# Optimization experiments

Hardware: AMD Instinct MI355X
Metric: run time of the kernel (lower is better)

Reference implementation:

```python
import jax, jax.numpy as jnp
import numpy as np

B, S, D, H = 2, 2048, 512, 8
HD = D // H
EPS = 1e-8
SCALE = HD ** -0.5


def setup_inputs() -> dict:
    key = jax.random.key(0)
    ks = jax.random.split(key, 12)
    gene_emb = jax.random.normal(ks[0], (B, S, D), jnp.float32)
    expr_emb = jax.random.normal(ks[1], (B, S, D), jnp.float32)
    M = jax.random.randint(ks[2], (B, S, S), 0, 2).astype(jnp.float32)
    def lin(k, fan_in, fan_out):
        kw, kb = jax.random.split(k)
        bound = 1.0 / np.sqrt(fan_in)
        W = jax.random.uniform(kw, (fan_in, fan_out), jnp.float32, -bound, bound)
        b = jax.random.uniform(kb, (fan_out,), jnp.float32, -bound, bound)
        return W, b
    Wf, bf = lin(ks[3], 2 * D, D)  # fused_emb_proj
    Wq, bq = lin(ks[4], D, D)
    Wk, bk = lin(ks[5], D, D)
    Wv, bv = lin(ks[6], D, D)
    Wo, bo = lin(ks[7], D, D)
    return {"gene_emb": gene_emb, "expr_emb": expr_emb, "M": M,
            "Wf": Wf, "bf": bf, "Wq": Wq, "bq": bq, "Wk": Wk, "bk": bk,
            "Wv": Wv, "bv": bv, "Wo": Wo, "bo": bo}


def reference(gene_emb, expr_emb, M, Wf, bf, Wq, bq, Wk, bk, Wv, bv, Wo, bo):
    # fused=True, self_attention=False path: Q and K from projected concat
    fused = jnp.concatenate([gene_emb, expr_emb], axis=-1) @ Wf + bf  # [B,S,D]
    Q = (fused @ Wq + bq).reshape(B, S, H, HD)
    K = (fused @ Wk + bk).reshape(B, S, H, HD)
    V = (expr_emb @ Wv + bv).reshape(B, S, H, HD)
    scores = jnp.einsum('bqhd,bkhd->bhqk', Q, K) * SCALE  # [B,H,S,S]
    Mh = M[:, None, :, :]  # broadcast over heads
    scores = scores + jnp.where(Mh == 0, -1e9, 0.0)
    attn = jax.nn.softmax(scores, axis=-1)
    A = attn * Mh  # gated weights
    A = A / (jnp.sum(jnp.abs(A), axis=-1, keepdims=True) + EPS)  # abs-sum renorm
    out = jnp.einsum('bhqk,bkhd->bqhd', A, V).reshape(B, S, D)
    return out @ Wo + bo
```

## Files before the change

### kernel.cpp

```cpp
#include <hip/hip_runtime.h>
#include <stdint.h>
#include <math.h>

#define BB 2
#define SS 2048
#define DDIM 512
#define HH 8
#define HDD 64
static constexpr float SCALE = 0.125f;

typedef unsigned short u16;
typedef short bf16x8 __attribute__((ext_vector_type(8)));
typedef float f32x4 __attribute__((ext_vector_type(4)));

__device__ __forceinline__ u16 f2bf(float x) {
  unsigned int u = __float_as_uint(x);
  unsigned int r = (u + 0x7fffu + ((u >> 16) & 1u)) >> 16;
  return (u16)r;
}

__device__ __forceinline__ void cp16(const void* g, void* l) {
  __builtin_amdgcn_global_load_lds(
      (const __attribute__((address_space(1))) void*)g,
      (__attribute__((address_space(3))) void*)l, 16, 0, 0);
}

__global__ __launch_bounds__(256) void cast_bf16_k(
    const float* __restrict__ g, const float* __restrict__ e,
    u16* __restrict__ og, u16* __restrict__ oe) {
  int i = blockIdx.x * 256 + threadIdx.x;
  float4 a = ((const float4*)g)[i];
  float4 b = ((const float4*)e)[i];
  ushort4 ua, ub;
  ua.x = f2bf(a.x); ua.y = f2bf(a.y); ua.z = f2bf(a.z); ua.w = f2bf(a.w);
  ub.x = f2bf(b.x); ub.y = f2bf(b.y); ub.z = f2bf(b.z); ub.w = f2bf(b.w);
  ((ushort4*)og)[i] = ua;
  ((ushort4*)oe)[i] = ub;
}

__global__ __launch_bounds__(256) void wprep_k(
    const float* __restrict__ Wf, const float* __restrict__ Wq,
    const float* __restrict__ Wk, const float* __restrict__ Wv,
    const float* __restrict__ Wo,
    u16* __restrict__ WfT, u16* __restrict__ WqT, u16* __restrict__ WkT,
    u16* __restrict__ WvT, u16* __restrict__ WoT) {
  int z = blockIdx.z;
  const float* W; u16* WT; int K;
  switch (z) {
    case 0: W = Wf; WT = WfT; K = 1024; break;
    case 1: W = Wq; WT = WqT; K = 512; break;
    case 2: W = Wk; WT = WkT; K = 512; break;
    case 3: W = Wv; WT = WvT; K = 512; break;
    default: W = Wo; WT = WoT; K = 512; break;
  }
  int k0 = blockIdx.y * 32;
  if (k0 >= K) return;
  int n0 = blockIdx.x * 32;
  __shared__ float t[32][33];
  int tx = threadIdx.x & 31, ty = threadIdx.x >> 5;
#pragma unroll
  for (int i = 0; i < 32; i += 8)
    t[ty + i][tx] = W[(size_t)(k0 + ty + i) * DDIM + n0 + tx];
  __syncthreads();
#pragma unroll
  for (int i = 0; i < 32; i += 8)
    WT[(size_t)(n0 + ty + i) * K + k0 + tx] = f2bf(t[tx][ty + i]);
}

template <int EPI>
__global__ __launch_bounds__(256) void gemm_k(
    const u16* __restrict__ A0, const u16* __restrict__ A1,
    const u16* __restrict__ Bt0, const u16* __restrict__ Bt1,
    const u16* __restrict__ Bt2,
    const float* __restrict__ bias0, const float* __restrict__ bias1,
    const float* __restrict__ bias2,
    u16* __restrict__ O0, u16* __restrict__ O1, u16* __restrict__ O2,
    float* __restrict__ OF) {
  constexpr int BK = 32;
  __shared__ alignas(16) u16 Al[128 * BK];
  __shared__ alignas(16) u16 Bl[64 * BK];

  const int tid = threadIdx.x;
  const int l = tid & 63, w = tid >> 6, lg = l >> 4, lr = l & 15;
  const int wm = w >> 1, wn = w & 1;
  const int m0 = blockIdx.y * 128;
  const int n0 = blockIdx.x * 64;
  const int Ksz = (EPI == 0) ? 1024 : 512;

  const u16* Aa = A0; const u16* Bt = Bt0; const float* bias = bias0;
  int z = 0;
  if (EPI == 1) {
    z = blockIdx.z;
    Aa = (z == 2) ? A1 : A0;
    Bt = (z == 0) ? Bt0 : (z == 1) ? Bt1 : Bt2;
    bias = (z == 0) ? bias0 : (z == 1) ? bias1 : bias2;
  }

  f32x4 zero4 = {0.f, 0.f, 0.f, 0.f};
  f32x4 acc[4][2];
#pragma unroll
  for (int i = 0; i < 4; ++i)
#pragma unroll
    for (int j = 0; j < 2; ++j) acc[i][j] = zero4;

  const int arow = tid >> 2;
  const int apos = tid & 3;

  for (int k0 = 0; k0 < Ksz; k0 += BK) {
    __syncthreads();
#pragma unroll
    for (int c = 0; c < 2; ++c) {
      int row = arow + 64 * c;
      int k8 = apos ^ ((row >> 1) & 3);
      int kg = k0 + 8 * k8;
      const u16* src;
      if (EPI == 0) {
        src = (kg < 512) ? (A0 + (size_t)(m0 + row) * 512 + kg)
                         : (A1 + (size_t)(m0 + row) * 512 + (kg - 512));
      } else {
        src = Aa + (size_t)(m0 + row) * 512 + kg;
      }
      cp16(src, (char*)Al + (size_t)row * 64 + apos * 16);
    }
    {
      int row = arow;
      int k8 = apos ^ ((row >> 1) & 3);
      const u16* src = Bt + (size_t)(n0 + row) * Ksz + k0 + 8 * k8;
      cp16(src, (char*)Bl + (size_t)row * 64 + apos * 16);
    }
    asm volatile("s_waitcnt vmcnt(0)" ::: "memory");
    __syncthreads();

    bf16x8 af[4], bfr[2];
#pragma unroll
    for (int i = 0; i < 4; ++i) {
      int row = 64 * wm + 16 * i + lr;
      af[i] = *(const bf16x8*)((const char*)Al + row * 64 +
                               ((lg ^ ((row >> 1) & 3)) * 16));
    }
#pragma unroll
    for (int j = 0; j < 2; ++j) {
      int row = 32 * wn + 16 * j + lr;
      bfr[j] = *(const bf16x8*)((const char*)Bl + row * 64 +
                                ((lg ^ ((row >> 1) & 3)) * 16));
    }
#pragma unroll
    for (int i = 0; i < 4; ++i)
#pragma unroll
      for (int j = 0; j < 2; ++j)
        acc[i][j] =
            __builtin_amdgcn_mfma_f32_16x16x32_bf16(af[i], bfr[j], acc[i][j], 0, 0, 0);
  }

#pragma unroll
  for (int j = 0; j < 2; ++j) {
    int c = n0 + 32 * wn + 16 * j + lr;
    float bv = bias[c];
#pragma unroll
    for (int i = 0; i < 4; ++i) {
      int qb = m0 + 64 * wm + 16 * i + 4 * lg;
      if (EPI == 0) {
#pragma unroll
        for (int r = 0; r < 4; ++r)
          O0[(size_t)(qb + r) * 512 + c] = f2bf(acc[i][j][r] + bv);
      } else if (EPI == 2) {
#pragma unroll
        for (int r = 0; r < 4; ++r)
          OF[(size_t)(qb + r) * 512 + c] = acc[i][j][r] + bv;
      } else {
        int b = qb >> 11, s = qb & 2047;
        int hh = c >> 6, hd = c & 63;
        if (z < 2) {
          u16* O = (z == 0) ? O0 : O1;
#pragma unroll
          for (int r = 0; r < 4; ++r)
            O[((size_t)(b * HH + hh) * SS + s + r) * HDD + hd] =
                f2bf(acc[i][j][r] + bv);
        } else {
          ushort4 v;
          v.x = f2bf(acc[i][j][0] + bv);
          v.y = f2bf(acc[i][j][1] + bv);
          v.z = f2bf(acc[i][j][2] + bv);
          v.w = f2bf(acc[i][j][3] + bv);
          *(ushort4*)(O2 + ((size_t)(b * HH + hh) * HDD + hd) * SS + s) = v;
        }
      }
    }
  }
}

__global__ __launch_bounds__(256) void attn_k(
    const u16* __restrict__ Qh, const u16* __restrict__ Kh,
    const u16* __restrict__ Vt, const float* __restrict__ Mm,
    u16* __restrict__ AO) {
  __shared__ alignas(16) u16 Kl[64 * 64];
  __shared__ alignas(16) u16 Vl[64 * 64];
  __shared__ alignas(16) u16 Pl[4][16 * 64];

  const int tid = threadIdx.x;
  const int l = tid & 63, w = tid >> 6, lg = l >> 4, lr = l & 15;
  const int bh = blockIdx.y, b = bh >> 3, h = bh & 7;
  const int qw = blockIdx.x * 64 + 16 * w;

  bf16x8 qf[2];
  {
    const u16* qp = Qh + ((size_t)bh * SS + qw + lr) * HDD + 8 * lg;
    qf[0] = *(const bf16x8*)qp;
    qf[1] = *(const bf16x8*)(qp + 32);
  }
  f32x4 zero4 = {0.f, 0.f, 0.f, 0.f};
  f32x4 o[4];
#pragma unroll
  for (int t = 0; t < 4; ++t) o[t] = zero4;
  float mrun[4] = {-INFINITY, -INFINITY, -INFINITY, -INFINITY};
  float lrun[4] = {0.f, 0.f, 0.f, 0.f};

  const float* Mb = Mm + ((size_t)b * SS + qw + 4 * lg) * SS;

  const int srow = tid >> 3;
  const int spos = tid & 7;

  for (int kt = 0; kt < SS / 64; ++kt) {
    const int kb = kt * 64;
    __syncthreads();
#pragma unroll
    for (int c = 0; c < 2; ++c) {
      int row = srow + 32 * c;
      int k8 = spos ^ (row & 7);
      size_t off = (size_t)tid * 16 + (size_t)c * 4096;
      cp16(Kh + ((size_t)bh * SS + kb + row) * HDD + 8 * k8, (char*)Kl + off);
      cp16(Vt + ((size_t)bh * HDD + row) * SS + kb + 8 * k8, (char*)Vl + off);
    }
    asm volatile("s_waitcnt vmcnt(0)" ::: "memory");
    __syncthreads();

    f32x4 sc[4];
#pragma unroll
    for (int ct = 0; ct < 4; ++ct) {
      int krow = 16 * ct + lr;
      const char* kbase = (const char*)Kl + krow * 128;
      bf16x8 k0f = *(const bf16x8*)(kbase + ((lg) ^ (krow & 7)) * 16);
      bf16x8 k1f = *(const bf16x8*)(kbase + ((4 + lg) ^ (krow & 7)) * 16);
      f32x4 zz = zero4;
      zz = __builtin_amdgcn_mfma_f32_16x16x32_bf16(qf[0], k0f, zz, 0, 0, 0);
      zz = __builtin_amdgcn_mfma_f32_16x16x32_bf16(qf[1], k1f, zz, 0, 0, 0);
      sc[ct] = zz;
    }
#pragma unroll
    for (int ct = 0; ct < 4; ++ct) {
#pragma unroll
      for (int r = 0; r < 4; ++r) {
        float mv = Mb[(size_t)r * SS + kb + 16 * ct + lr];
        sc[ct][r] = (mv != 0.0f) ? sc[ct][r] * SCALE : -INFINITY;
      }
    }
#pragma unroll
    for (int r = 0; r < 4; ++r) {
      float t = fmaxf(fmaxf(sc[0][r], sc[1][r]), fmaxf(sc[2][r], sc[3][r]));
      t = fmaxf(t, __shfl_xor(t, 1));
      t = fmaxf(t, __shfl_xor(t, 2));
      t = fmaxf(t, __shfl_xor(t, 4));
      t = fmaxf(t, __shfl_xor(t, 8));
      float mnew = fmaxf(mrun[r], t);
      float fac = (mnew == -INFINITY) ? 1.0f : __expf(mrun[r] - mnew);
      float psum = 0.f;
#pragma unroll
      for (int ct = 0; ct < 4; ++ct) {
        float p = (sc[ct][r] == -INFINITY) ? 0.f : __expf(sc[ct][r] - mnew);
        sc[ct][r] = p;
        psum += p;
      }
      psum += __shfl_xor(psum, 1);
      psum += __shfl_xor(psum, 2);
      psum += __shfl_xor(psum, 4);
      psum += __shfl_xor(psum, 8);
      mrun[r] = mnew;
      lrun[r] = lrun[r] * fac + psum;
#pragma unroll
      for (int t4 = 0; t4 < 4; ++t4) o[t4][r] *= fac;
    }
    u16* Pw = Pl[w];
#pragma unroll
    for (int ct = 0; ct < 4; ++ct) {
#pragma unroll
      for (int r = 0; r < 4; ++r) {
        int row = 4 * lg + r;
        int col = 16 * ct + lr;
        int pos = (col >> 3) ^ (row & 7);
        Pw[row * 64 + pos * 8 + (col & 7)] = f2bf(sc[ct][r]);
      }
    }
#pragma unroll
    for (int kk = 0; kk < 2; ++kk) {
      bf16x8 pf = *(const bf16x8*)((const char*)Pw + lr * 128 +
                                   (((4 * kk + lg) ^ (lr & 7)) * 16));
#pragma unroll
      for (int t4 = 0; t4 < 4; ++t4) {
        int vrow = 16 * t4 + lr;
        bf16x8 vf = *(const bf16x8*)((const char*)Vl + vrow * 128 +
                                     (((4 * kk + lg) ^ (vrow & 7)) * 16));
        o[t4] = __builtin_amdgcn_mfma_f32_16x16x32_bf16(pf, vf, o[t4], 0, 0, 0);
      }
    }
  }

#pragma unroll
  for (int r = 0; r < 4; ++r) {
    float inv = (lrun[r] > 0.f) ? 1.0f / (lrun[r] + 1e-8f) : 0.f;
    size_t row = (size_t)b * SS + qw + 4 * lg + r;
#pragma unroll
    for (int t4 = 0; t4 < 4; ++t4) {
      int d = 16 * t4 + lr;
      AO[row * DDIM + h * HDD + d] = f2bf(o[t4][r] * inv);
    }
  }
}

extern "C" void kernel_launch(void* const* d_in, const int* in_sizes, int n_in,
                              void* d_out, int out_size, void* d_ws, size_t ws_size,
                              hipStream_t stream) {
  if (ws_size < (size_t)(31.5 * 1024 * 1024)) return;

  const float* gene = (const float*)d_in[0];
  const float* expr = (const float*)d_in[1];
  const float* Mm = (const float*)d_in[2];
  const float* Wf = (const float*)d_in[3];
  const float* bf = (const float*)d_in[4];
  const float* Wq = (const float*)d_in[5];
  const float* bq = (const float*)d_in[6];
  const float* Wk = (const float*)d_in[7];
  const float* bk = (const float*)d_in[8];
  const float* Wv = (const float*)d_in[9];
  const float* bv = (const float*)d_in[10];
  const float* Wo = (const float*)d_in[11];
  const float* bo = (const float*)d_in[12];
  float* out = (float*)d_out;

  char* ws = (char*)d_ws;
  const size_t MB4 = 4194304;
  u16* geneB = (u16*)(ws + 0 * MB4);
  u16* exprB = (u16*)(ws + 1 * MB4);
  u16* fusedB = (u16*)(ws + 2 * MB4);
  u16* QhB = (u16*)(ws + 3 * MB4);
  u16* KhB = (u16*)(ws + 4 * MB4);
  u16* VtB = (u16*)(ws + 5 * MB4);
  u16* attnB = (u16*)(ws + 6 * MB4);
  u16* WfT = (u16*)(ws + 7 * MB4);
  u16* WqT = (u16*)(ws + 7 * MB4 + 1048576);
  u16* WkT = (u16*)(ws + 7 * MB4 + 1048576 + 524288);
  u16* WvT = (u16*)(ws + 7 * MB4 + 1048576 + 2 * 524288);
  u16* WoT = (u16*)(ws + 7 * MB4 + 1048576 + 3 * 524288);

  cast_bf16_k<<<2048, 256, 0, stream>>>(gene, expr, geneB, exprB);
  wprep_k<<<dim3(16, 32, 5), 256, 0, stream>>>(Wf, Wq, Wk, Wv, Wo, WfT, WqT,
                                               WkT, WvT, WoT);
  gemm_k<0><<<dim3(8, 32), 256, 0, stream>>>(geneB, exprB, WfT, nullptr, nullptr,
                                             bf, nullptr, nullptr, fusedB,
                                             nullptr, nullptr, nullptr);
  gemm_k<1><<<dim3(8, 32, 3), 256, 0, stream>>>(fusedB, exprB, WqT, WkT, WvT,
                                                bq, bk, bv, QhB, KhB, VtB,
                                                nullptr);
  attn_k<<<dim3(32, 16), 256, 0, stream>>>(QhB, KhB, VtB, Mm, attnB);
  gemm_k<2><<<dim3(8, 32), 256, 0, stream>>>(attnB, nullptr, WoT, nullptr,
                                             nullptr, bo, nullptr, nullptr,
                                             nullptr, nullptr, nullptr, out);
}
```

Baseline: 229.7 us.

## Split attention keys across two wave groups and shrink GEMM M-tile to 64

The attention kernel now runs 512 threads per block. Two groups of four waves each handle half of the key sequence, and their running max, sum and output accumulators are merged through shared memory at the end. This doubles in-flight work per query tile without adding blocks, which targets latency and occupancy limits in the 512-block attention grid. The GEMMs also drop from a 128-row to a 64-row M tile, doubling grid size for better CU fill at the cost of more B-tile reloads.

```diff
diff --git a/kernel.cpp b/kernel.cpp
--- a/kernel.cpp
+++ b/kernel.cpp
@@ -77,13 +77,13 @@
     u16* __restrict__ O0, u16* __restrict__ O1, u16* __restrict__ O2,
     float* __restrict__ OF) {
   constexpr int BK = 32;
-  __shared__ alignas(16) u16 Al[128 * BK];
+  __shared__ alignas(16) u16 Al[64 * BK];
   __shared__ alignas(16) u16 Bl[64 * BK];
 
   const int tid = threadIdx.x;
   const int l = tid & 63, w = tid >> 6, lg = l >> 4, lr = l & 15;
   const int wm = w >> 1, wn = w & 1;
-  const int m0 = blockIdx.y * 128;
+  const int m0 = blockIdx.y * 64;
   const int n0 = blockIdx.x * 64;
   const int Ksz = (EPI == 0) ? 1024 : 512;
 
@@ -97,44 +97,40 @@
   }
 
   f32x4 zero4 = {0.f, 0.f, 0.f, 0.f};
-  f32x4 acc[4][2];
-#pragma unroll
-  for (int i = 0; i < 4; ++i)
+  f32x4 acc[2][2];
+#pragma unroll
+  for (int i = 0; i < 2; ++i)
 #pragma unroll
     for (int j = 0; j < 2; ++j) acc[i][j] = zero4;
 
   const int arow = tid >> 2;
   const int apos = tid & 3;
+  const int k8s = apos ^ ((arow >> 1) & 3);
 
   for (int k0 = 0; k0 < Ksz; k0 += BK) {
     __syncthreads();
-#pragma unroll
-    for (int c = 0; c < 2; ++c) {
-      int row = arow + 64 * c;
-      int k8 = apos ^ ((row >> 1) & 3);
-      int kg = k0 + 8 * k8;
+    {
+      int kg = k0 + 8 * k8s;
       const u16* src;
       if (EPI == 0) {
-        src = (kg < 512) ? (A0 + (size_t)(m0 + row) * 512 + kg)
-                         : (A1 + (size_t)(m0 + row) * 512 + (kg - 512));
+        src = (kg < 512) ? (A0 + (size_t)(m0 + arow) * 512 + kg)
+                         : (A1 + (size_t)(m0 + arow) * 512 + (kg - 512));
       } else {
-        src = Aa + (size_t)(m0 + row) * 512 + kg;
-      }
-      cp16(src, (char*)Al + (size_t)row * 64 + apos * 16);
+        src = Aa + (size_t)(m0 + arow) * 512 + kg;
+      }
+      cp16(src, (char*)Al + (size_t)arow * 64 + apos * 16);
     }
     {
-      int row = arow;
-      int k8 = apos ^ ((row >> 1) & 3);
-      const u16* src = Bt + (size_t)(n0 + row) * Ksz + k0 + 8 * k8;
-      cp16(src, (char*)Bl + (size_t)row * 64 + apos * 16);
+      const u16* src = Bt + (size_t)(n0 + arow) * Ksz + k0 + 8 * k8s;
+      cp16(src, (char*)Bl + (size_t)arow * 64 + apos * 16);
     }
     asm volatile("s_waitcnt vmcnt(0)" ::: "memory");
     __syncthreads();
 
-    bf16x8 af[4], bfr[2];
-#pragma unroll
-    for (int i = 0; i < 4; ++i) {
-      int row = 64 * wm + 16 * i + lr;
+    bf16x8 af[2], bfr[2];
+#pragma unroll
+    for (int i = 0; i < 2; ++i) {
+      int row = 32 * wm + 16 * i + lr;
       af[i] = *(const bf16x8*)((const char*)Al + row * 64 +
                                ((lg ^ ((row >> 1) & 3)) * 16));
     }
@@ -145,7 +141,7 @@
                                 ((lg ^ ((row >> 1) & 3)) * 16));
     }
 #pragma unroll
-    for (int i = 0; i < 4; ++i)
+    for (int i = 0; i < 2; ++i)
 #pragma unroll
       for (int j = 0; j < 2; ++j)
         acc[i][j] =
@@ -157,8 +153,8 @@
     int c = n0 + 32 * wn + 16 * j + lr;
     float bv = bias[c];
 #pragma unroll
-    for (int i = 0; i < 4; ++i) {
-      int qb = m0 + 64 * wm + 16 * i + 4 * lg;
+    for (int i = 0; i < 2; ++i) {
+      int qb = m0 + 32 * wm + 16 * i + 4 * lg;
       if (EPI == 0) {
 #pragma unroll
         for (int r = 0; r < 4; ++r)
@@ -189,18 +185,19 @@
   }
 }
 
-__global__ __launch_bounds__(256) void attn_k(
+__global__ __launch_bounds__(512) void attn2_k(
     const u16* __restrict__ Qh, const u16* __restrict__ Kh,
     const u16* __restrict__ Vt, const float* __restrict__ Mm,
     u16* __restrict__ AO) {
-  __shared__ alignas(16) u16 Kl[64 * 64];
-  __shared__ alignas(16) u16 Vl[64 * 64];
-  __shared__ alignas(16) u16 Pl[4][16 * 64];
+  __shared__ alignas(16) u16 Kl[2][64 * 64];
+  __shared__ alignas(16) u16 Vl[2][64 * 64];
+  __shared__ alignas(16) u16 Pl[8][16 * 64];
 
   const int tid = threadIdx.x;
   const int l = tid & 63, w = tid >> 6, lg = l >> 4, lr = l & 15;
+  const int qg = w & 3, kh = w >> 2;
   const int bh = blockIdx.y, b = bh >> 3, h = bh & 7;
-  const int qw = blockIdx.x * 64 + 16 * w;
+  const int qw = blockIdx.x * 64 + 16 * qg;
 
   bf16x8 qf[2];
   {
@@ -219,26 +216,28 @@
 
   const int srow = tid >> 3;
   const int spos = tid & 7;
-
-  for (int kt = 0; kt < SS / 64; ++kt) {
-    const int kb = kt * 64;
+  const int sk8 = spos ^ (srow & 7);
+  const size_t sdst = (size_t)tid * 16;
+
+  for (int kt = 0; kt < 16; ++kt) {
+    const int kb0 = kt * 64, kb1 = 1024 + kt * 64;
     __syncthreads();
-#pragma unroll
-    for (int c = 0; c < 2; ++c) {
-      int row = srow + 32 * c;
-      int k8 = spos ^ (row & 7);
-      size_t off = (size_t)tid * 16 + (size_t)c * 4096;
-      cp16(Kh + ((size_t)bh * SS + kb + row) * HDD + 8 * k8, (char*)Kl + off);
-      cp16(Vt + ((size_t)bh * HDD + row) * SS + kb + 8 * k8, (char*)Vl + off);
-    }
+    cp16(Kh + ((size_t)bh * SS + kb0 + srow) * HDD + 8 * sk8, (char*)Kl[0] + sdst);
+    cp16(Vt + ((size_t)bh * HDD + srow) * SS + kb0 + 8 * sk8, (char*)Vl[0] + sdst);
+    cp16(Kh + ((size_t)bh * SS + kb1 + srow) * HDD + 8 * sk8, (char*)Kl[1] + sdst);
+    cp16(Vt + ((size_t)bh * HDD + srow) * SS + kb1 + 8 * sk8, (char*)Vl[1] + sdst);
     asm volatile("s_waitcnt vmcnt(0)" ::: "memory");
     __syncthreads();
 
+    const int kb = kh * 1024 + kt * 64;
+    const u16* Klw = Kl[kh];
+    const u16* Vlw = Vl[kh];
+
     f32x4 sc[4];
 #pragma unroll
     for (int ct = 0; ct < 4; ++ct) {
       int krow = 16 * ct + lr;
-      const char* kbase = (const char*)Kl + krow * 128;
+      const char* kbase = (const char*)Klw + krow * 128;
       bf16x8 k0f = *(const bf16x8*)(kbase + ((lg) ^ (krow & 7)) * 16);
       bf16x8 k1f = *(const bf16x8*)(kbase + ((4 + lg) ^ (krow & 7)) * 16);
       f32x4 zz = zero4;
@@ -297,21 +296,41 @@
 #pragma unroll
       for (int t4 = 0; t4 < 4; ++t4) {
         int vrow = 16 * t4 + lr;
-        bf16x8 vf = *(const bf16x8*)((const char*)Vl + vrow * 128 +
+        bf16x8 vf = *(const bf16x8*)((const char*)Vlw + vrow * 128 +
                                      (((4 * kk + lg) ^ (vrow & 7)) * 16));
         o[t4] = __builtin_amdgcn_mfma_f32_16x16x32_bf16(pf, vf, o[t4], 0, 0, 0);
       }
     }
   }
 
-#pragma unroll
-  for (int r = 0; r < 4; ++r) {
-    float inv = (lrun[r] > 0.f) ? 1.0f / (lrun[r] + 1e-8f) : 0.f;
-    size_t row = (size_t)b * SS + qw + 4 * lg + r;
-#pragma unroll
-    for (int t4 = 0; t4 < 4; ++t4) {
-      int d = 16 * t4 + lr;
-      AO[row * DDIM + h * HDD + d] = f2bf(o[t4][r] * inv);
+  __syncthreads();
+  float* sh = (float*)Kl;
+  if (kh == 1) {
+    float* p = sh + ((size_t)(w - 4) * 64 + l) * 24;
+#pragma unroll
+    for (int r = 0; r < 4; ++r) { p[r] = mrun[r]; p[4 + r] = lrun[r]; }
+#pragma unroll
+    for (int t4 = 0; t4 < 4; ++t4)
+#pragma unroll
+      for (int r = 0; r < 4; ++r) p[8 + 4 * t4 + r] = o[t4][r];
+  }
+  __syncthreads();
+  if (kh == 0) {
+    const float* p = sh + ((size_t)w * 64 + l) * 24;
+#pragma unroll
+    for (int r = 0; r < 4; ++r) {
+      float mB = p[r], lB = p[4 + r];
+      float ms = fmaxf(mrun[r], mB);
+      float fa = (mrun[r] > -INFINITY) ? __expf(mrun[r] - ms) : 0.f;
+      float fb = (mB > -INFINITY) ? __expf(mB - ms) : 0.f;
+      float ls = lrun[r] * fa + lB * fb;
+      float inv = (ls > 0.f) ? 1.0f / (ls + 1e-8f) : 0.f;
+      size_t row = (size_t)b * SS + qw + 4 * lg + r;
+#pragma unroll
+      for (int t4 = 0; t4 < 4; ++t4) {
+        float ov = o[t4][r] * fa + p[8 + 4 * t4 + r] * fb;
+        AO[row * DDIM + h * HDD + 16 * t4 + lr] = f2bf(ov * inv);
+      }
     }
   }
 }
@@ -354,14 +373,14 @@
   cast_bf16_k<<<2048, 256, 0, stream>>>(gene, expr, geneB, exprB);
   wprep_k<<<dim3(16, 32, 5), 256, 0, stream>>>(Wf, Wq, Wk, Wv, Wo, WfT, WqT,
                                                WkT, WvT, WoT);
-  gemm_k<0><<<dim3(8, 32), 256, 0, stream>>>(geneB, exprB, WfT, nullptr, nullptr,
+  gemm_k<0><<<dim3(8, 64), 256, 0, stream>>>(geneB, exprB, WfT, nullptr, nullptr,
                                              bf, nullptr, nullptr, fusedB,
                                              nullptr, nullptr, nullptr);
-  gemm_k<1><<<dim3(8, 32, 3), 256, 0, stream>>>(fusedB, exprB, WqT, WkT, WvT,
+  gemm_k<1><<<dim3(8, 64, 3), 256, 0, stream>>>(fusedB, exprB, WqT, WkT, WvT,
                                                 bq, bk, bv, QhB, KhB, VtB,
                                                 nullptr);
-  attn_k<<<dim3(32, 16), 256, 0, stream>>>(QhB, KhB, VtB, Mm, attnB);
-  gemm_k<2><<<dim3(8, 32), 256, 0, stream>>>(attnB, nullptr, WoT, nullptr,
+  attn2_k<<<dim3(32, 16), 512, 0, stream>>>(QhB, KhB, VtB, Mm, attnB);
+  gemm_k<2><<<dim3(8, 64), 256, 0, stream>>>(attnB, nullptr, WoT, nullptr,
                                              nullptr, bo, nullptr, nullptr,
                                              nullptr, nullptr, nullptr, out);
 }
```

New measurement: 225.2 us. 1.02x faster.
